# Optimization experiments

Measured on AMD Instinct MI355X. Metric: run time of the kernel, lower is better.

Reference implementation:

```python
import jax, jax.numpy as jnp
import numpy as np

N_QUBITS = 12
N_LAYERS = 6
BATCH = 256
INPUT_DIM = 256
OUT_DIM = 64
PI = float(np.pi)


def _ry_mat(a):
    # a: scalar or (B,) real angle -> (...,2,2) complex64 RY matrix
    c, s = jnp.cos(a * 0.5), jnp.sin(a * 0.5)
    return jnp.stack([jnp.stack([c, -s], -1), jnp.stack([s, c], -1)], -2).astype(jnp.complex64)


def _rz_mat(a):
    # diag(e^{-i a/2}, e^{+i a/2})
    em = jnp.exp(-0.5j * a.astype(jnp.complex64))
    ep = jnp.exp(0.5j * a.astype(jnp.complex64))
    z = jnp.zeros_like(em)
    return jnp.stack([jnp.stack([em, z], -1), jnp.stack([z, ep], -1)], -2)


def _apply_1q(state, U, w):
    # shared (2,2) gate on wire w; state: (B, 2, ..., 2)
    s = jnp.moveaxis(state, w + 1, -1)
    s = jnp.einsum('ij,b...j->b...i', U, s)
    return jnp.moveaxis(s, -1, w + 1)


def _apply_1q_batched(state, U, w):
    # per-sample (B,2,2) gate on wire w
    s = jnp.moveaxis(state, w + 1, -1)
    s = jnp.einsum('bij,b...j->b...i', U, s)
    return jnp.moveaxis(s, -1, w + 1)


def _cnot(state, c, t):
    s0 = jnp.take(state, 0, axis=c + 1)
    s1 = jnp.take(state, 1, axis=c + 1)
    t_ax = t + 1 if t < c else t  # target axis index after removing control axis
    s1 = jnp.flip(s1, axis=t_ax)
    return jnp.stack([s0, s1], axis=c + 1)


def _cz(state, c, t):
    idx = [slice(None)] * (N_QUBITS + 1)
    idx[c + 1] = 1
    idx[t + 1] = 1
    return state.at[tuple(idx)].multiply(-1.0)


def _run_circuit(xq, q_weights):
    # xq: (B, n_qubits) in [-1,1]; forward passes xq*pi, circuit multiplies by pi again
    B = xq.shape[0]
    enc = xq * (PI * PI)
    state = jnp.zeros((B, 2 ** N_QUBITS), jnp.complex64).at[:, 0].set(1.0)
    state = state.reshape((B,) + (2,) * N_QUBITS)
    for i in range(N_QUBITS):
        state = _apply_1q_batched(state, _ry_mat(enc[:, i]), i)
    w = q_weights.reshape(N_LAYERS, N_QUBITS, 3)
    for layer in range(N_LAYERS):
        for i in range(N_QUBITS):
            # PennyLane order: RZ(w0) then RY(w1) then RZ(w2) -> U = RZ2 @ RY1 @ RZ0
            U = _rz_mat(w[layer, i, 2]) @ _ry_mat(w[layer, i, 1]) @ _rz_mat(w[layer, i, 0])
            state = _apply_1q(state, U, i)
        for i in range(N_QUBITS):
            state = _cnot(state, i, (i + 1) % N_QUBITS)
        if layer % 2 == 0 and layer < N_LAYERS - 1:
            for i in range(N_QUBITS):
                state = _apply_1q_batched(state, _ry_mat(enc[:, i] * 0.5), i)
        if layer % 2 == 1:
            for i in range(0, N_QUBITS - 2, 2):
                state = _cz(state, i, i + 2)
    # PauliZ expectation on wires 0,1,2
    p = (state.real ** 2 + state.imag ** 2).reshape(B, 2, 2, 2, -1).sum(-1)  # (B,2,2,2)
    z0 = (p[:, 0] - p[:, 1]).sum((-1, -2))
    z1 = (p[:, :, 0] - p[:, :, 1]).sum((-1, -2))
    z2 = (p[:, :, :, 0] - p[:, :, :, 1]).sum((-1, -2))
    return jnp.stack([z0, z1, z2], -1)  # (B, 3) float32


def _layernorm(h, g, b, eps=1e-5):
    mu = h.mean(-1, keepdims=True)
    var = ((h - mu) ** 2).mean(-1, keepdims=True)
    return (h - mu) * jax.lax.rsqrt(var + eps) * g + b


def _forward(x, W1, b1, g_ln, b_ln, W2, b2, W3, b3, q_weights, W4, b4, W5, b5):
    gelu = lambda t: jax.nn.gelu(t, approximate=False)
    h = gelu(x @ W1.T + b1)
    h = _layernorm(h, g_ln, b_ln)
    h = gelu(h @ W2.T + b2)
    xq = jnp.tanh(h @ W3.T + b3)  # (B, n_qubits)
    q = _run_circuit(xq, q_weights)  # (B, 3)
    return gelu(q @ W4.T + b4) @ W5.T + b5  # (B, OUT_DIM)


def setup_inputs() -> dict:
    key = jax.random.key(0)
    ks = jax.random.split(key, 8)
    rn = lambda k, shape, s=0.05: (jax.random.normal(k, shape) * s).astype(jnp.float32)
    return {
        'x': jax.random.normal(ks[0], (BATCH, INPUT_DIM), jnp.float32),
        'W1': rn(ks[1], (128, INPUT_DIM)), 'b1': jnp.zeros(128, jnp.float32),
        'g_ln': jnp.ones(128, jnp.float32), 'b_ln': jnp.zeros(128, jnp.float32),
        'W2': rn(ks[2], (64, 128)), 'b2': jnp.zeros(64, jnp.float32),
        'W3': rn(ks[3], (N_QUBITS, 64)), 'b3': jnp.zeros(N_QUBITS, jnp.float32),
        'q_weights': (jax.random.normal(ks[4], (N_LAYERS * N_QUBITS * 3,)) * 0.1).astype(jnp.float32),
        'W4': rn(ks[5], (32, 3)), 'b4': jnp.zeros(32, jnp.float32),
        'W5': rn(ks[6], (OUT_DIM, 32)), 'b5': jnp.zeros(OUT_DIM, jnp.float32),
    }


def reference(x, W1, b1, g_ln, b_ln, W2, b2, W3, b3, q_weights, W4, b4, W5, b5):
    return _forward(x, W1, b1, g_ln, b_ln, W2, b2, W3, b3, q_weights, W4, b4, W5, b5)
```

## Files before the change

### kernel.cpp

```cpp
#include <hip/hip_runtime.h>
#include <math.h>

#define NQ   12
#define NL   6
#define BATCH 256
#define NT   512
#define PI2  9.869604401089358f

typedef float v2f __attribute__((ext_vector_type(2)));

__device__ __forceinline__ float geluf(float x) {
    return 0.5f * x * (1.0f + erff(x * 0.70710678118654752f));
}

__device__ __forceinline__ int Pad(int x) { return x + (x >> 4) + (x >> 8); }

__device__ __forceinline__ int gmap(int j) {
    return ((j ^ (j >> 1)) & 0x3FF)
         | ((((j >> 10) ^ (j >> 11) ^ j) & 1) << 10)
         | ((((j >> 11) ^ j) & 1) << 11);
}

__device__ __forceinline__ v2f mk2(float a, float b) { v2f r; r.x = a; r.y = b; return r; }
__device__ __forceinline__ v2f spl(float s)          { v2f r; r.x = s; r.y = s; return r; }
__device__ __forceinline__ v2f swn(v2f x)            { v2f r; r.x = -x.y; r.y = x.x; return r; }
__device__ __forceinline__ v2f cml(v2f u, v2f x)          { return spl(u.x) * x + spl(u.y) * swn(x); }
__device__ __forceinline__ v2f cma(v2f u, v2f x, v2f acc) { return acc + spl(u.x) * x + spl(u.y) * swn(x); }

__device__ __forceinline__ void bf(v2f& x0, v2f& x1, const v2f* U) {
    v2f o0 = cma(U[1], x1, cml(U[0], x0));
    v2f o1 = cma(U[3], x1, cml(U[2], x0));
    x0 = o0; x1 = o1;
}

__device__ __forceinline__ void gate_reg(v2f* a, const v2f* U, int bit) {
    #pragma unroll
    for (int m = 0; m < 8; m++) {
        if (m & bit) continue;
        bf(a[m], a[m | bit], U);
    }
}

template<int CTRL>
__device__ __forceinline__ v2f dppv(v2f v) {
    int x = __builtin_amdgcn_update_dpp(0, __float_as_int(v.x), CTRL, 0xF, 0xF, true);
    int y = __builtin_amdgcn_update_dpp(0, __float_as_int(v.y), CTRL, 0xF, 0xF, true);
    return mk2(__int_as_float(x), __int_as_float(y));
}
template<int CTRL>
__device__ __forceinline__ void gate_dpp(v2f* a, const v2f* U, bool sel) {
    const v2f cA = sel ? U[3] : U[0];
    const v2f cB = sel ? U[2] : U[1];
    #pragma unroll
    for (int m = 0; m < 8; m++) {
        v2f v = dppv<CTRL>(a[m]);
        a[m] = cma(cB, v, cml(cA, a[m]));
    }
}

__global__ __launch_bounds__(NT)
void qpu_kernel(const float* __restrict__ x,   const float* __restrict__ W1, const float* __restrict__ b1,
                const float* __restrict__ g_ln, const float* __restrict__ b_ln,
                const float* __restrict__ W2,  const float* __restrict__ b2,
                const float* __restrict__ W3,  const float* __restrict__ b3,
                const float* __restrict__ qw,  const float* __restrict__ W4, const float* __restrict__ b4,
                const float* __restrict__ W5,  const float* __restrict__ b5,
                float* __restrict__ out)
{
    __shared__ v2f   bufA[4368];
    __shared__ v2f   bufB[4368];
    __shared__ v2f   Um[NL * NQ * 4];
    __shared__ float xs[256];
    __shared__ float pr[1280];
    __shared__ float h1n[128];
    __shared__ float h2s[64];
    __shared__ float xqs[NQ];
    __shared__ float musd[2];
    __shared__ float qv[3];
    __shared__ float h4s[32];
    __shared__ float zred[8][3];

    const int t = threadIdx.x;
    const int b = blockIdx.x;

    if (t < 256) xs[t] = x[b * 256 + t];
    __syncthreads();

    {
        const int o = t >> 2, part = t & 3;
        const float4* w  = (const float4*)(W1 + o * 256) + part * 16;
        const float*  xp = xs + part * 64;
        float a0 = 0.f, a1 = 0.f, a2 = 0.f, a3 = 0.f;
        #pragma unroll
        for (int k = 0; k < 16; k++) {
            float4 wv = w[k];
            a0 = fmaf(wv.x, xp[4 * k + 0], a0);
            a1 = fmaf(wv.y, xp[4 * k + 1], a1);
            a2 = fmaf(wv.z, xp[4 * k + 2], a2);
            a3 = fmaf(wv.w, xp[4 * k + 3], a3);
        }
        pr[o * 5 + part] = (a0 + a1) + (a2 + a3);
    }
    __syncthreads();
    if (t < 128) {
        float s = pr[t * 5 + 0] + pr[t * 5 + 1] + pr[t * 5 + 2] + pr[t * 5 + 3];
        h1n[t] = geluf(s + b1[t]);
    }
    __syncthreads();

    if (t < 64) {
        float v0 = h1n[t], v1 = h1n[t + 64];
        float s1 = v0 + v1;
        float s2 = fmaf(v0, v0, v1 * v1);
        #pragma unroll
        for (int off = 32; off > 0; off >>= 1) {
            s1 += __shfl_down(s1, off);
            s2 += __shfl_down(s2, off);
        }
        if (t == 0) {
            float mu  = s1 * (1.f / 128.f);
            float var = s2 * (1.f / 128.f) - mu * mu;
            musd[0] = mu;
            musd[1] = rsqrtf(var + 1e-5f);
        }
    }
    __syncthreads();
    if (t < 128) h1n[t] = (h1n[t] - musd[0]) * musd[1] * g_ln[t] + b_ln[t];
    __syncthreads();

    {
        const int o = t >> 3, part = t & 7;
        if (o < 64) {
            const float4* w  = (const float4*)(W2 + o * 128) + part * 4;
            const float*  hp = h1n + part * 16;
            float a0 = 0.f, a1 = 0.f, a2 = 0.f, a3 = 0.f;
            #pragma unroll
            for (int k = 0; k < 4; k++) {
                float4 wv = w[k];
                a0 = fmaf(wv.x, hp[4 * k + 0], a0);
                a1 = fmaf(wv.y, hp[4 * k + 1], a1);
                a2 = fmaf(wv.z, hp[4 * k + 2], a2);
                a3 = fmaf(wv.w, hp[4 * k + 3], a3);
            }
            pr[o * 9 + part] = (a0 + a1) + (a2 + a3);
        }
    }
    __syncthreads();
    if (t < 64) {
        float s = 0.f;
        #pragma unroll
        for (int k = 0; k < 8; k++) s += pr[t * 9 + k];
        h2s[t] = geluf(s + b2[t]);
    }
    __syncthreads();

    if (t < 96) {
        const int o = t >> 3, part = t & 7;
        const float4* w  = (const float4*)(W3 + o * 64) + part * 2;
        const float*  hp = h2s + part * 8;
        float4 w0 = w[0], w1 = w[1];
        float s = 0.f;
        s = fmaf(w0.x, hp[0], s); s = fmaf(w0.y, hp[1], s);
        s = fmaf(w0.z, hp[2], s); s = fmaf(w0.w, hp[3], s);
        s = fmaf(w1.x, hp[4], s); s = fmaf(w1.y, hp[5], s);
        s = fmaf(w1.z, hp[6], s); s = fmaf(w1.w, hp[7], s);
        pr[o * 9 + part] = s;
    }
    __syncthreads();
    if (t < NQ) {
        float s = 0.f;
        #pragma unroll
        for (int k = 0; k < 8; k++) s += pr[t * 9 + k];
        xqs[t] = tanhf(s + b3[t]);
    }
    __syncthreads();

    if (t < NL * NQ) {
        const int l = t / NQ;
        const int i = t % NQ;
        float a  = qw[t * 3 + 0];
        float bb = qw[t * 3 + 1];
        float c  = qw[t * 3 + 2];
        float sb, cb;   sincosf(0.5f * bb, &sb, &cb);
        float apc = 0.5f * (a + c), amc = 0.5f * (a - c);
        float sapc, capc; sincosf(apc, &sapc, &capc);
        float samc, camc; sincosf(amc, &samc, &camc);
        float u00x =  cb * capc, u00y = -cb * sapc;
        float u01x = -sb * camc, u01y = -sb * samc;
        float u10x =  sb * camc, u10y = -sb * samc;
        float u11x =  cb * capc, u11y =  cb * sapc;

        float theta = 0.f;
        bool merge = false;
        if (l == 0)      { theta = xqs[i] * PI2;        merge = true; }
        else if (l & 1)  { theta = xqs[i] * PI2 * 0.5f; merge = true; }
        if (merge) {
            float sy, cy; sincosf(0.5f * theta, &sy, &cy);
            float m00x = u00x * cy + u01x * sy, m00y = u00y * cy + u01y * sy;
            float m01x = -u00x * sy + u01x * cy, m01y = -u00y * sy + u01y * cy;
            float m10x = u10x * cy + u11x * sy, m10y = u10y * cy + u11y * sy;
            float m11x = -u10x * sy + u11x * cy, m11y = -u10y * sy + u11y * cy;
            u00x = m00x; u00y = m00y; u01x = m01x; u01y = m01y;
            u10x = m10x; u10y = m10y; u11x = m11x; u11y = m11y;
        }
        Um[t * 4 + 0] = mk2(u00x, u00y);
        Um[t * 4 + 1] = mk2(u01x, u01y);
        Um[t * 4 + 2] = mk2(u10x, u10y);
        Um[t * 4 + 3] = mk2(u11x, u11y);
    }
    __syncthreads();

    const int PwA = 8 * t + (t >> 1) + (t >> 5);
    const int s0  = (((t     ) & 1) << 9) | (((t >> 1) & 1) << 10) | ((t >> 2) & 1)
                  | (((t >> 3) & 1) << 11) | (((t >> 4) & 1) << 1)  | (((t >> 5) & 1) << 2)
                  | (((t >> 6) & 1) << 3)  | (((t >> 7) & 1) << 4)  | (((t >> 8) & 1) << 6);
    const int Ps  = Pad(s0);
    const int g8  = gmap(8 * t);

    v2f a[8];
    {
        v2f common = Um[(11 - 3) * 4 + ((g8 >> 3) & 1) * 2];
        #pragma unroll
        for (int k = 4; k <= 9; k++) {
            common = cml(common, Um[(11 - k) * 4 + ((g8 >> k) & 1) * 2]);
        }
        #pragma unroll
        for (int m = 0; m < 8; m++) {
            const int gmc = (m ^ (m >> 1)) | ((m & 1) ? 0xC00 : 0);
            const int g = g8 ^ gmc;
            v2f v = common;
            v = cml(v, Um[11 * 4 + ((g     ) & 1) * 2]);
            v = cml(v, Um[10 * 4 + ((g >> 1) & 1) * 2]);
            v = cml(v, Um[ 9 * 4 + ((g >> 2) & 1) * 2]);
            v = cml(v, Um[ 1 * 4 + ((g >> 10) & 1) * 2]);
            v = cml(v, Um[ 0 * 4 + ((g >> 11) & 1) * 2]);
            a[m] = v;
        }
    }

    const bool d1 = t & 1, d2 = t & 2, d8 = t & 8;
    #pragma unroll 1
    for (int l = 1; l < NL; l++) {
        const v2f* UL = &Um[l * NQ * 4];

        gate_reg(a, &UL[11 * 4], 1);
        gate_reg(a, &UL[10 * 4], 2);
        gate_reg(a, &UL[ 9 * 4], 4);
        gate_dpp<0xB1> (a, &UL[8 * 4], d1);
        gate_dpp<0x4E> (a, &UL[7 * 4], d2);
        gate_dpp<0x128>(a, &UL[5 * 4], d8);

        #pragma unroll
        for (int m = 0; m < 8; m++) bufB[PwA + m] = a[m];
        __syncthreads();
        #pragma unroll
        for (int m = 0; m < 8; m++) {
            const int dm = 34 * (m & 1) + 136 * ((m >> 1) & 1) + 273 * ((m >> 2) & 1);
            a[m] = bufB[Ps + dm];
        }

        gate_reg(a, &UL[6 * 4], 1);
        gate_reg(a, &UL[4 * 4], 2);
        gate_reg(a, &UL[3 * 4], 4);
        gate_dpp<0xB1> (a, &UL[2 * 4], d1);
        gate_dpp<0x4E> (a, &UL[1 * 4], d2);
        gate_dpp<0x128>(a, &UL[0 * 4], d8);

        if (l < NL - 1) {
            #pragma unroll
            for (int m = 0; m < 8; m++) {
                const int dm = 34 * (m & 1) + 136 * ((m >> 1) & 1) + 273 * ((m >> 2) & 1);
                bufA[Ps + dm] = a[m];
            }
            __syncthreads();
            const bool czl = (l == 1) || (l == 3);
            #pragma unroll
            for (int m = 0; m < 8; m++) {
                const int gmc = (m ^ (m >> 1)) | ((m & 1) ? 0xC00 : 0);
                const int g = g8 ^ gmc;
                v2f v = bufA[Pad(g)];
                const int j = 8 * t + m;
                if (czl && (__popc(j & (j << 2) & 0xAA8) & 1)) v = -v;
                a[m] = v;
            }
        }
    }

    float alt = 0.f, tot = 0.f;
    #pragma unroll
    for (int m = 0; m < 8; m++) {
        float p = a[m].x * a[m].x + a[m].y * a[m].y;
        tot += p;
        alt += (__popc(m) & 1) ? -p : p;
    }
    float z0 = (__popc(t & 0x1F7) & 1) ? -alt : alt;
    float z1 = (__popc(t & 0x00A) & 1) ? -tot : tot;
    float z2 = (__popc(t & 0x00B) & 1) ? -tot : tot;

    #pragma unroll
    for (int off = 32; off > 0; off >>= 1) {
        z0 += __shfl_down(z0, off);
        z1 += __shfl_down(z1, off);
        z2 += __shfl_down(z2, off);
    }
    if ((t & 63) == 0) {
        zred[t >> 6][0] = z0;
        zred[t >> 6][1] = z1;
        zred[t >> 6][2] = z2;
    }
    __syncthreads();
    if (t == 0) {
        float q0 = 0.f, q1 = 0.f, q2 = 0.f;
        #pragma unroll
        for (int w = 0; w < 8; w++) {
            q0 += zred[w][0]; q1 += zred[w][1]; q2 += zred[w][2];
        }
        qv[0] = q0; qv[1] = q1; qv[2] = q2;
    }
    __syncthreads();

    if (t < 32) {
        float h = b4[t];
        h = fmaf(qv[0], W4[t * 3 + 0], h);
        h = fmaf(qv[1], W4[t * 3 + 1], h);
        h = fmaf(qv[2], W4[t * 3 + 2], h);
        h4s[t] = geluf(h);
    }
    __syncthreads();
    if (t < 64) {
        float acc = b5[t];
        #pragma unroll
        for (int h = 0; h < 32; h++) acc = fmaf(h4s[h], W5[t * 32 + h], acc);
        out[b * 64 + t] = acc;
    }
}

extern "C" void kernel_launch(void* const* d_in, const int* in_sizes, int n_in,
                              void* d_out, int out_size, void* d_ws, size_t ws_size,
                              hipStream_t stream) {
    (void)in_sizes; (void)n_in; (void)d_ws; (void)ws_size; (void)out_size;
    const float* x    = (const float*)d_in[0];
    const float* W1   = (const float*)d_in[1];
    const float* b1   = (const float*)d_in[2];
    const float* g_ln = (const float*)d_in[3];
    const float* b_ln = (const float*)d_in[4];
    const float* W2   = (const float*)d_in[5];
    const float* b2   = (const float*)d_in[6];
    const float* W3   = (const float*)d_in[7];
    const float* b3   = (const float*)d_in[8];
    const float* qw   = (const float*)d_in[9];
    const float* W4   = (const float*)d_in[10];
    const float* b4   = (const float*)d_in[11];
    const float* W5   = (const float*)d_in[12];
    const float* b5   = (const float*)d_in[13];
    float* out = (float*)d_out;

    qpu_kernel<<<BATCH, NT, 0, stream>>>(x, W1, b1, g_ln, b_ln, W2, b2,
                                         W3, b3, qw, W4, b4, W5, b5, out);
}
```

Baseline: 108.3 us.

## Double threads to 1024 with 4 amplitudes per thread in split real/imag layout

```diff
diff --git a/kernel.cpp b/kernel.cpp
--- a/kernel.cpp
+++ b/kernel.cpp
@@ -4,7 +4,7 @@
 #define NQ   12
 #define NL   6
 #define BATCH 256
-#define NT   512
+#define NT   1024
 #define PI2  9.869604401089358f
 
 typedef float v2f __attribute__((ext_vector_type(2)));
@@ -21,41 +21,16 @@
          | ((((j >> 11) ^ j) & 1) << 11);
 }
 
-__device__ __forceinline__ v2f mk2(float a, float b) { v2f r; r.x = a; r.y = b; return r; }
-__device__ __forceinline__ v2f spl(float s)          { v2f r; r.x = s; r.y = s; return r; }
-__device__ __forceinline__ v2f swn(v2f x)            { v2f r; r.x = -x.y; r.y = x.x; return r; }
-__device__ __forceinline__ v2f cml(v2f u, v2f x)          { return spl(u.x) * x + spl(u.y) * swn(x); }
-__device__ __forceinline__ v2f cma(v2f u, v2f x, v2f acc) { return acc + spl(u.x) * x + spl(u.y) * swn(x); }
-
-__device__ __forceinline__ void bf(v2f& x0, v2f& x1, const v2f* U) {
-    v2f o0 = cma(U[1], x1, cml(U[0], x0));
-    v2f o1 = cma(U[3], x1, cml(U[2], x0));
-    x0 = o0; x1 = o1;
-}
-
-__device__ __forceinline__ void gate_reg(v2f* a, const v2f* U, int bit) {
-    #pragma unroll
-    for (int m = 0; m < 8; m++) {
-        if (m & bit) continue;
-        bf(a[m], a[m | bit], U);
-    }
-}
-
 template<int CTRL>
 __device__ __forceinline__ v2f dppv(v2f v) {
     int x = __builtin_amdgcn_update_dpp(0, __float_as_int(v.x), CTRL, 0xF, 0xF, true);
     int y = __builtin_amdgcn_update_dpp(0, __float_as_int(v.y), CTRL, 0xF, 0xF, true);
-    return mk2(__int_as_float(x), __int_as_float(y));
-}
-template<int CTRL>
-__device__ __forceinline__ void gate_dpp(v2f* a, const v2f* U, bool sel) {
-    const v2f cA = sel ? U[3] : U[0];
-    const v2f cB = sel ? U[2] : U[1];
-    #pragma unroll
-    for (int m = 0; m < 8; m++) {
-        v2f v = dppv<CTRL>(a[m]);
-        a[m] = cma(cB, v, cml(cA, a[m]));
-    }
+    v2f r; r.x = __int_as_float(x); r.y = __int_as_float(y); return r;
+}
+__device__ __forceinline__ v2f swz4(v2f v) {
+    int x = __builtin_amdgcn_ds_swizzle(__float_as_int(v.x), 0x101F);
+    int y = __builtin_amdgcn_ds_swizzle(__float_as_int(v.y), 0x101F);
+    v2f r; r.x = __int_as_float(x); r.y = __int_as_float(y); return r;
 }
 
 __global__ __launch_bounds__(NT)
@@ -67,18 +42,18 @@
                 const float* __restrict__ W5,  const float* __restrict__ b5,
                 float* __restrict__ out)
 {
-    __shared__ v2f   bufA[4368];
-    __shared__ v2f   bufB[4368];
-    __shared__ v2f   Um[NL * NQ * 4];
-    __shared__ float xs[256];
-    __shared__ float pr[1280];
-    __shared__ float h1n[128];
-    __shared__ float h2s[64];
-    __shared__ float xqs[NQ];
-    __shared__ float musd[2];
-    __shared__ float qv[3];
-    __shared__ float h4s[32];
-    __shared__ float zred[8][3];
+    __shared__ float2 bufA[4368];
+    __shared__ float2 bufB[4368];
+    __shared__ float  Um8[NL * NQ * 8];
+    __shared__ float  xs[256];
+    __shared__ float  pr[1280];
+    __shared__ float  h1n[128];
+    __shared__ float  h2s[64];
+    __shared__ float  xqs[NQ];
+    __shared__ float  musd[2];
+    __shared__ float  qv[3];
+    __shared__ float  h4s[32];
+    __shared__ float  zred[16][3];
 
     const int t = threadIdx.x;
     const int b = blockIdx.x;
@@ -87,23 +62,25 @@
     __syncthreads();
 
     {
-        const int o = t >> 2, part = t & 3;
-        const float4* w  = (const float4*)(W1 + o * 256) + part * 16;
-        const float*  xp = xs + part * 64;
+        const int o = t >> 3, part = t & 7;
+        const float4* w  = (const float4*)(W1 + o * 256) + part * 8;
+        const float*  xp = xs + part * 32;
         float a0 = 0.f, a1 = 0.f, a2 = 0.f, a3 = 0.f;
         #pragma unroll
-        for (int k = 0; k < 16; k++) {
+        for (int k = 0; k < 8; k++) {
             float4 wv = w[k];
             a0 = fmaf(wv.x, xp[4 * k + 0], a0);
             a1 = fmaf(wv.y, xp[4 * k + 1], a1);
             a2 = fmaf(wv.z, xp[4 * k + 2], a2);
             a3 = fmaf(wv.w, xp[4 * k + 3], a3);
         }
-        pr[o * 5 + part] = (a0 + a1) + (a2 + a3);
+        pr[o * 9 + part] = (a0 + a1) + (a2 + a3);
     }
     __syncthreads();
     if (t < 128) {
-        float s = pr[t * 5 + 0] + pr[t * 5 + 1] + pr[t * 5 + 2] + pr[t * 5 + 3];
+        float s = 0.f;
+        #pragma unroll
+        for (int k = 0; k < 8; k++) s += pr[t * 9 + k];
         h1n[t] = geluf(s + b1[t]);
     }
     __syncthreads();
@@ -128,22 +105,20 @@
     if (t < 128) h1n[t] = (h1n[t] - musd[0]) * musd[1] * g_ln[t] + b_ln[t];
     __syncthreads();
 
-    {
+    if (t < 512) {
         const int o = t >> 3, part = t & 7;
-        if (o < 64) {
-            const float4* w  = (const float4*)(W2 + o * 128) + part * 4;
-            const float*  hp = h1n + part * 16;
-            float a0 = 0.f, a1 = 0.f, a2 = 0.f, a3 = 0.f;
-            #pragma unroll
-            for (int k = 0; k < 4; k++) {
-                float4 wv = w[k];
-                a0 = fmaf(wv.x, hp[4 * k + 0], a0);
-                a1 = fmaf(wv.y, hp[4 * k + 1], a1);
-                a2 = fmaf(wv.z, hp[4 * k + 2], a2);
-                a3 = fmaf(wv.w, hp[4 * k + 3], a3);
-            }
-            pr[o * 9 + part] = (a0 + a1) + (a2 + a3);
-        }
+        const float4* w  = (const float4*)(W2 + o * 128) + part * 4;
+        const float*  hp = h1n + part * 16;
+        float a0 = 0.f, a1 = 0.f, a2 = 0.f, a3 = 0.f;
+        #pragma unroll
+        for (int k = 0; k < 4; k++) {
+            float4 wv = w[k];
+            a0 = fmaf(wv.x, hp[4 * k + 0], a0);
+            a1 = fmaf(wv.y, hp[4 * k + 1], a1);
+            a2 = fmaf(wv.z, hp[4 * k + 2], a2);
+            a3 = fmaf(wv.w, hp[4 * k + 3], a3);
+        }
+        pr[o * 9 + part] = (a0 + a1) + (a2 + a3);
     }
     __syncthreads();
     if (t < 64) {
@@ -196,106 +171,172 @@
         else if (l & 1)  { theta = xqs[i] * PI2 * 0.5f; merge = true; }
         if (merge) {
             float sy, cy; sincosf(0.5f * theta, &sy, &cy);
-            float m00x = u00x * cy + u01x * sy, m00y = u00y * cy + u01y * sy;
+            float m00x = u00x * cy + u01x * sy,  m00y = u00y * cy + u01y * sy;
             float m01x = -u00x * sy + u01x * cy, m01y = -u00y * sy + u01y * cy;
-            float m10x = u10x * cy + u11x * sy, m10y = u10y * cy + u11y * sy;
+            float m10x = u10x * cy + u11x * sy,  m10y = u10y * cy + u11y * sy;
             float m11x = -u10x * sy + u11x * cy, m11y = -u10y * sy + u11y * cy;
             u00x = m00x; u00y = m00y; u01x = m01x; u01y = m01y;
             u10x = m10x; u10y = m10y; u11x = m11x; u11y = m11y;
         }
-        Um[t * 4 + 0] = mk2(u00x, u00y);
-        Um[t * 4 + 1] = mk2(u01x, u01y);
-        Um[t * 4 + 2] = mk2(u10x, u10y);
-        Um[t * 4 + 3] = mk2(u11x, u11y);
-    }
-    __syncthreads();
-
-    const int PwA = 8 * t + (t >> 1) + (t >> 5);
-    const int s0  = (((t     ) & 1) << 9) | (((t >> 1) & 1) << 10) | ((t >> 2) & 1)
-                  | (((t >> 3) & 1) << 11) | (((t >> 4) & 1) << 1)  | (((t >> 5) & 1) << 2)
-                  | (((t >> 6) & 1) << 3)  | (((t >> 7) & 1) << 4)  | (((t >> 8) & 1) << 6);
+        float* d = &Um8[t * 8];
+        d[0] = u00x; d[1] = u00y; d[2] = u01x; d[3] = u01y;
+        d[4] = u10x; d[5] = u10y; d[6] = u11x; d[7] = u11y;
+    }
+    __syncthreads();
+
+    const int PwA = 4 * t + (t >> 2) + (t >> 6);
+    const int s0  = ((t >> 4) & 3) | (((t >> 6) & 15) << 2) | ((t & 15) << 8);
     const int Ps  = Pad(s0);
-    const int g8  = gmap(8 * t);
-
-    v2f a[8];
+    const int g4t = gmap(4 * t);
+    const int pg0 = Pad(g4t);
+    const int pg1 = Pad(g4t ^ 0xC01);
+    const int pg2 = Pad(g4t ^ 0x003);
+    const int pg3 = Pad(g4t ^ 0xC02);
+    const int  czb = __popc(t & (t >> 2) & 0xAA) & 1;
+    const float sA = czb ? -1.f : 1.f;
+    const float sB = (czb ^ ((t >> 1) & 1)) ? -1.f : 1.f;
+    const bool d1 = t & 1, d2 = t & 2, d4 = t & 4, d8 = t & 8;
+
+    v2f R01, R23, I01, I23;
     {
-        v2f common = Um[(11 - 3) * 4 + ((g8 >> 3) & 1) * 2];
-        #pragma unroll
-        for (int k = 4; k <= 9; k++) {
-            common = cml(common, Um[(11 - k) * 4 + ((g8 >> k) & 1) * 2]);
-        }
-        #pragma unroll
-        for (int m = 0; m < 8; m++) {
-            const int gmc = (m ^ (m >> 1)) | ((m & 1) ? 0xC00 : 0);
-            const int g = g8 ^ gmc;
-            v2f v = common;
-            v = cml(v, Um[11 * 4 + ((g     ) & 1) * 2]);
-            v = cml(v, Um[10 * 4 + ((g >> 1) & 1) * 2]);
-            v = cml(v, Um[ 9 * 4 + ((g >> 2) & 1) * 2]);
-            v = cml(v, Um[ 1 * 4 + ((g >> 10) & 1) * 2]);
-            v = cml(v, Um[ 0 * 4 + ((g >> 11) & 1) * 2]);
-            a[m] = v;
-        }
-    }
-
-    const bool d1 = t & 1, d2 = t & 2, d8 = t & 8;
+        float cr, ci;
+        {
+            const float* u = &Um8[9 * 8 + (((g4t >> 2) & 1) << 2)];
+            cr = u[0]; ci = u[1];
+        }
+        #pragma unroll
+        for (int k = 3; k <= 9; k++) {
+            const float* u = &Um8[(11 - k) * 8 + (((g4t >> k) & 1) << 2)];
+            float nr = cr * u[0] - ci * u[1];
+            float ni = cr * u[1] + ci * u[0];
+            cr = nr; ci = ni;
+        }
+        const int GM[4] = {0, 0xC01, 0x003, 0xC02};
+        float vr[4], vi[4];
+        #pragma unroll
+        for (int m = 0; m < 4; m++) {
+            const int g = g4t ^ GM[m];
+            float rr = cr, ii = ci;
+            const float* u0 = &Um8[11 * 8 + ((g & 1) << 2)];
+            const float* u1 = &Um8[10 * 8 + (((g >> 1) & 1) << 2)];
+            const float* ua = &Um8[ 1 * 8 + (((g >> 10) & 1) << 2)];
+            const float* ub = &Um8[ 0 * 8 + (((g >> 11) & 1) << 2)];
+            float nr, ni;
+            nr = rr * u0[0] - ii * u0[1]; ni = rr * u0[1] + ii * u0[0]; rr = nr; ii = ni;
+            nr = rr * u1[0] - ii * u1[1]; ni = rr * u1[1] + ii * u1[0]; rr = nr; ii = ni;
+            nr = rr * ua[0] - ii * ua[1]; ni = rr * ua[1] + ii * ua[0]; rr = nr; ii = ni;
+            nr = rr * ub[0] - ii * ub[1]; ni = rr * ub[1] + ii * ub[0]; rr = nr; ii = ni;
+            vr[m] = rr; vi[m] = ii;
+        }
+        R01.x = vr[0]; R01.y = vr[1]; R23.x = vr[2]; R23.y = vr[3];
+        I01.x = vi[0]; I01.y = vi[1]; I23.x = vi[2]; I23.y = vi[3];
+    }
+
     #pragma unroll 1
     for (int l = 1; l < NL; l++) {
-        const v2f* UL = &Um[l * NQ * 4];
-
-        gate_reg(a, &UL[11 * 4], 1);
-        gate_reg(a, &UL[10 * 4], 2);
-        gate_reg(a, &UL[ 9 * 4], 4);
-        gate_dpp<0xB1> (a, &UL[8 * 4], d1);
-        gate_dpp<0x4E> (a, &UL[7 * 4], d2);
-        gate_dpp<0x128>(a, &UL[5 * 4], d8);
-
-        #pragma unroll
-        for (int m = 0; m < 8; m++) bufB[PwA + m] = a[m];
+        const float* UL = &Um8[l * NQ * 8];
+
+        {
+            const float* u = &UL[11 * 8];
+            float r0 = R01.x, i0 = I01.x, r1 = R01.y, i1 = I01.y;
+            R01.x = u[0]*r0 - u[1]*i0 + u[2]*r1 - u[3]*i1;
+            I01.x = u[0]*i0 + u[1]*r0 + u[2]*i1 + u[3]*r1;
+            R01.y = u[4]*r0 - u[5]*i0 + u[6]*r1 - u[7]*i1;
+            I01.y = u[4]*i0 + u[5]*r0 + u[6]*i1 + u[7]*r1;
+            r0 = R23.x; i0 = I23.x; r1 = R23.y; i1 = I23.y;
+            R23.x = u[0]*r0 - u[1]*i0 + u[2]*r1 - u[3]*i1;
+            I23.x = u[0]*i0 + u[1]*r0 + u[2]*i1 + u[3]*r1;
+            R23.y = u[4]*r0 - u[5]*i0 + u[6]*r1 - u[7]*i1;
+            I23.y = u[4]*i0 + u[5]*r0 + u[6]*i1 + u[7]*r1;
+        }
+        {
+            const float* u = &UL[10 * 8];
+            v2f r0 = u[0]*R01 - u[1]*I01 + u[2]*R23 - u[3]*I23;
+            v2f i0 = u[0]*I01 + u[1]*R01 + u[2]*I23 + u[3]*R23;
+            v2f r1 = u[4]*R01 - u[5]*I01 + u[6]*R23 - u[7]*I23;
+            v2f i1 = u[4]*I01 + u[5]*R01 + u[6]*I23 + u[7]*R23;
+            R01 = r0; I01 = i0; R23 = r1; I23 = i1;
+        }
+        #define LANE_GATE(PERM, Q, SEL) do {                                  \
+            const float* u = &UL[(Q) * 8];                                    \
+            float cAx = (SEL) ? u[6] : u[0], cAy = (SEL) ? u[7] : u[1];       \
+            float cBx = (SEL) ? u[4] : u[2], cBy = (SEL) ? u[5] : u[3];       \
+            v2f vR0 = PERM(R01), vI0 = PERM(I01);                             \
+            v2f vR1 = PERM(R23), vI1 = PERM(I23);                             \
+            v2f nR0 = cAx*R01 - cAy*I01 + cBx*vR0 - cBy*vI0;                  \
+            v2f nI0 = cAx*I01 + cAy*R01 + cBx*vI0 + cBy*vR0;                  \
+            v2f nR1 = cAx*R23 - cAy*I23 + cBx*vR1 - cBy*vI1;                  \
+            v2f nI1 = cAx*I23 + cAy*R23 + cBx*vI1 + cBy*vR1;                  \
+            R01 = nR0; I01 = nI0; R23 = nR1; I23 = nI1; } while (0)
+
+        LANE_GATE(dppv<0xB1>,  9, d1);
+        LANE_GATE(dppv<0x4E>,  8, d2);
+        LANE_GATE(swz4,        7, d4);
+        LANE_GATE(dppv<0x128>, 6, d8);
+
+        bufB[PwA + 0] = make_float2(R01.x, I01.x);
+        bufB[PwA + 1] = make_float2(R01.y, I01.y);
+        bufB[PwA + 2] = make_float2(R23.x, I23.x);
+        bufB[PwA + 3] = make_float2(R23.y, I23.y);
         __syncthreads();
-        #pragma unroll
-        for (int m = 0; m < 8; m++) {
-            const int dm = 34 * (m & 1) + 136 * ((m >> 1) & 1) + 273 * ((m >> 2) & 1);
-            a[m] = bufB[Ps + dm];
-        }
-
-        gate_reg(a, &UL[6 * 4], 1);
-        gate_reg(a, &UL[4 * 4], 2);
-        gate_reg(a, &UL[3 * 4], 4);
-        gate_dpp<0xB1> (a, &UL[2 * 4], d1);
-        gate_dpp<0x4E> (a, &UL[1 * 4], d2);
-        gate_dpp<0x128>(a, &UL[0 * 4], d8);
+        {
+            float2 v0 = bufB[Ps], v1 = bufB[Ps + 68], v2 = bufB[Ps + 136], v3 = bufB[Ps + 204];
+            R01.x = v0.x; I01.x = v0.y; R01.y = v1.x; I01.y = v1.y;
+            R23.x = v2.x; I23.x = v2.y; R23.y = v3.x; I23.y = v3.y;
+        }
+
+        {
+            const float* u = &UL[5 * 8];
+            float r0 = R01.x, i0 = I01.x, r1 = R01.y, i1 = I01.y;
+            R01.x = u[0]*r0 - u[1]*i0 + u[2]*r1 - u[3]*i1;
+            I01.x = u[0]*i0 + u[1]*r0 + u[2]*i1 + u[3]*r1;
+            R01.y = u[4]*r0 - u[5]*i0 + u[6]*r1 - u[7]*i1;
+            I01.y = u[4]*i0 + u[5]*r0 + u[6]*i1 + u[7]*r1;
+            r0 = R23.x; i0 = I23.x; r1 = R23.y; i1 = I23.y;
+            R23.x = u[0]*r0 - u[1]*i0 + u[2]*r1 - u[3]*i1;
+            I23.x = u[0]*i0 + u[1]*r0 + u[2]*i1 + u[3]*r1;
+            R23.y = u[4]*r0 - u[5]*i0 + u[6]*r1 - u[7]*i1;
+            I23.y = u[4]*i0 + u[5]*r0 + u[6]*i1 + u[7]*r1;
+        }
+        {
+            const float* u = &UL[4 * 8];
+            v2f r0 = u[0]*R01 - u[1]*I01 + u[2]*R23 - u[3]*I23;
+            v2f i0 = u[0]*I01 + u[1]*R01 + u[2]*I23 + u[3]*R23;
+            v2f r1 = u[4]*R01 - u[5]*I01 + u[6]*R23 - u[7]*I23;
+            v2f i1 = u[4]*I01 + u[5]*R01 + u[6]*I23 + u[7]*R23;
+            R01 = r0; I01 = i0; R23 = r1; I23 = i1;
+        }
+        LANE_GATE(dppv<0xB1>,  3, d1);
+        LANE_GATE(dppv<0x4E>,  2, d2);
+        LANE_GATE(swz4,        1, d4);
+        LANE_GATE(dppv<0x128>, 0, d8);
+        #undef LANE_GATE
 
         if (l < NL - 1) {
-            #pragma unroll
-            for (int m = 0; m < 8; m++) {
-                const int dm = 34 * (m & 1) + 136 * ((m >> 1) & 1) + 273 * ((m >> 2) & 1);
-                bufA[Ps + dm] = a[m];
+            bufA[Ps +   0] = make_float2(R01.x, I01.x);
+            bufA[Ps +  68] = make_float2(R01.y, I01.y);
+            bufA[Ps + 136] = make_float2(R23.x, I23.x);
+            bufA[Ps + 204] = make_float2(R23.y, I23.y);
+            __syncthreads();
+            float2 w0 = bufA[pg0], w1 = bufA[pg1], w2 = bufA[pg2], w3 = bufA[pg3];
+            if ((l == 1) || (l == 3)) {
+                w0.x *= sA; w0.y *= sA; w1.x *= sA; w1.y *= sA;
+                w2.x *= sB; w2.y *= sB; w3.x *= sB; w3.y *= sB;
             }
-            __syncthreads();
-            const bool czl = (l == 1) || (l == 3);
-            #pragma unroll
-            for (int m = 0; m < 8; m++) {
-                const int gmc = (m ^ (m >> 1)) | ((m & 1) ? 0xC00 : 0);
-                const int g = g8 ^ gmc;
-                v2f v = bufA[Pad(g)];
-                const int j = 8 * t + m;
-                if (czl && (__popc(j & (j << 2) & 0xAA8) & 1)) v = -v;
-                a[m] = v;
-            }
-        }
-    }
-
-    float alt = 0.f, tot = 0.f;
-    #pragma unroll
-    for (int m = 0; m < 8; m++) {
-        float p = a[m].x * a[m].x + a[m].y * a[m].y;
-        tot += p;
-        alt += (__popc(m) & 1) ? -p : p;
-    }
-    float z0 = (__popc(t & 0x1F7) & 1) ? -alt : alt;
-    float z1 = (__popc(t & 0x00A) & 1) ? -tot : tot;
-    float z2 = (__popc(t & 0x00B) & 1) ? -tot : tot;
+            R01.x = w0.x; I01.x = w0.y; R01.y = w1.x; I01.y = w1.y;
+            R23.x = w2.x; I23.x = w2.y; R23.y = w3.x; I23.y = w3.y;
+        }
+    }
+
+    float p0 = R01.x * R01.x + I01.x * I01.x;
+    float p1 = R01.y * R01.y + I01.y * I01.y;
+    float p2 = R23.x * R23.x + I23.x * I23.x;
+    float p3 = R23.y * R23.y + I23.y * I23.y;
+    float alt = (p0 - p1) - (p2 - p3);
+    float tot = (p0 + p1) + (p2 + p3);
+    float z0 = (__popc(t & 0x3F7) & 1) ? -alt : alt;
+    float z1 = (__popc(t & 0x00C) & 1) ? -tot : tot;
+    float z2 = (__popc(t & 0x00E) & 1) ? -tot : tot;
 
     #pragma unroll
     for (int off = 32; off > 0; off >>= 1) {
@@ -312,7 +353,7 @@
     if (t == 0) {
         float q0 = 0.f, q1 = 0.f, q2 = 0.f;
         #pragma unroll
-        for (int w = 0; w < 8; w++) {
+        for (int w = 0; w < 16; w++) {
             q0 += zred[w][0]; q1 += zred[w][1]; q2 += zred[w][2];
         }
         qv[0] = q0; qv[1] = q1; qv[2] = q2;
```

New measurement: 103.1 us. 4.8% less time.

## Store state as split real/imag packed vectors and prelayout gate matrices

Applied to the files above, without the earlier changes.

```diff
diff --git a/kernel.cpp b/kernel.cpp
--- a/kernel.cpp
+++ b/kernel.cpp
@@ -21,41 +21,16 @@
          | ((((j >> 11) ^ j) & 1) << 11);
 }
 
-__device__ __forceinline__ v2f mk2(float a, float b) { v2f r; r.x = a; r.y = b; return r; }
-__device__ __forceinline__ v2f spl(float s)          { v2f r; r.x = s; r.y = s; return r; }
-__device__ __forceinline__ v2f swn(v2f x)            { v2f r; r.x = -x.y; r.y = x.x; return r; }
-__device__ __forceinline__ v2f cml(v2f u, v2f x)          { return spl(u.x) * x + spl(u.y) * swn(x); }
-__device__ __forceinline__ v2f cma(v2f u, v2f x, v2f acc) { return acc + spl(u.x) * x + spl(u.y) * swn(x); }
-
-__device__ __forceinline__ void bf(v2f& x0, v2f& x1, const v2f* U) {
-    v2f o0 = cma(U[1], x1, cml(U[0], x0));
-    v2f o1 = cma(U[3], x1, cml(U[2], x0));
-    x0 = o0; x1 = o1;
-}
-
-__device__ __forceinline__ void gate_reg(v2f* a, const v2f* U, int bit) {
-    #pragma unroll
-    for (int m = 0; m < 8; m++) {
-        if (m & bit) continue;
-        bf(a[m], a[m | bit], U);
-    }
+__device__ __forceinline__ int sigma(int x) {
+    return ((x & 0x1E) << 6) | ((x & 0x780) >> 6)
+         | ((x & 0x41) << 5) | ((x & 0x820) >> 5);
 }
 
 template<int CTRL>
 __device__ __forceinline__ v2f dppv(v2f v) {
     int x = __builtin_amdgcn_update_dpp(0, __float_as_int(v.x), CTRL, 0xF, 0xF, true);
     int y = __builtin_amdgcn_update_dpp(0, __float_as_int(v.y), CTRL, 0xF, 0xF, true);
-    return mk2(__int_as_float(x), __int_as_float(y));
-}
-template<int CTRL>
-__device__ __forceinline__ void gate_dpp(v2f* a, const v2f* U, bool sel) {
-    const v2f cA = sel ? U[3] : U[0];
-    const v2f cB = sel ? U[2] : U[1];
-    #pragma unroll
-    for (int m = 0; m < 8; m++) {
-        v2f v = dppv<CTRL>(a[m]);
-        a[m] = cma(cB, v, cml(cA, a[m]));
-    }
+    v2f r; r.x = __int_as_float(x); r.y = __int_as_float(y); return r;
 }
 
 __global__ __launch_bounds__(NT)
@@ -67,18 +42,19 @@
                 const float* __restrict__ W5,  const float* __restrict__ b5,
                 float* __restrict__ out)
 {
-    __shared__ v2f   bufA[4368];
-    __shared__ v2f   bufB[4368];
-    __shared__ v2f   Um[NL * NQ * 4];
-    __shared__ float xs[256];
-    __shared__ float pr[1280];
-    __shared__ float h1n[128];
-    __shared__ float h2s[64];
-    __shared__ float xqs[NQ];
-    __shared__ float musd[2];
-    __shared__ float qv[3];
-    __shared__ float h4s[32];
-    __shared__ float zred[8][3];
+    __shared__ float2 bufA[4368];
+    __shared__ float2 bufB[4368];
+    __shared__ float  Umr[5 * 12 * 8];
+    __shared__ float4 L0c[12];
+    __shared__ float  xs[256];
+    __shared__ float  pr[1280];
+    __shared__ float  h1n[128];
+    __shared__ float  h2s[64];
+    __shared__ float  xqs[NQ];
+    __shared__ float  musd[2];
+    __shared__ float  qv[3];
+    __shared__ float  h4s[32];
+    __shared__ float  zred[8][3];
 
     const int t = threadIdx.x;
     const int b = blockIdx.x;
@@ -130,20 +106,18 @@
 
     {
         const int o = t >> 3, part = t & 7;
-        if (o < 64) {
-            const float4* w  = (const float4*)(W2 + o * 128) + part * 4;
-            const float*  hp = h1n + part * 16;
-            float a0 = 0.f, a1 = 0.f, a2 = 0.f, a3 = 0.f;
-            #pragma unroll
-            for (int k = 0; k < 4; k++) {
-                float4 wv = w[k];
-                a0 = fmaf(wv.x, hp[4 * k + 0], a0);
-                a1 = fmaf(wv.y, hp[4 * k + 1], a1);
-                a2 = fmaf(wv.z, hp[4 * k + 2], a2);
-                a3 = fmaf(wv.w, hp[4 * k + 3], a3);
-            }
-            pr[o * 9 + part] = (a0 + a1) + (a2 + a3);
-        }
+        const float4* w  = (const float4*)(W2 + o * 128) + part * 4;
+        const float*  hp = h1n + part * 16;
+        float a0 = 0.f, a1 = 0.f, a2 = 0.f, a3 = 0.f;
+        #pragma unroll
+        for (int k = 0; k < 4; k++) {
+            float4 wv = w[k];
+            a0 = fmaf(wv.x, hp[4 * k + 0], a0);
+            a1 = fmaf(wv.y, hp[4 * k + 1], a1);
+            a2 = fmaf(wv.z, hp[4 * k + 2], a2);
+            a3 = fmaf(wv.w, hp[4 * k + 3], a3);
+        }
+        pr[o * 9 + part] = (a0 + a1) + (a2 + a3);
     }
     __syncthreads();
     if (t < 64) {
@@ -196,103 +170,198 @@
         else if (l & 1)  { theta = xqs[i] * PI2 * 0.5f; merge = true; }
         if (merge) {
             float sy, cy; sincosf(0.5f * theta, &sy, &cy);
-            float m00x = u00x * cy + u01x * sy, m00y = u00y * cy + u01y * sy;
+            float m00x = u00x * cy + u01x * sy,  m00y = u00y * cy + u01y * sy;
             float m01x = -u00x * sy + u01x * cy, m01y = -u00y * sy + u01y * cy;
-            float m10x = u10x * cy + u11x * sy, m10y = u10y * cy + u11y * sy;
+            float m10x = u10x * cy + u11x * sy,  m10y = u10y * cy + u11y * sy;
             float m11x = -u10x * sy + u11x * cy, m11y = -u10y * sy + u11y * cy;
             u00x = m00x; u00y = m00y; u01x = m01x; u01y = m01y;
             u10x = m10x; u10y = m10y; u11x = m11x; u11y = m11y;
         }
-        Um[t * 4 + 0] = mk2(u00x, u00y);
-        Um[t * 4 + 1] = mk2(u01x, u01y);
-        Um[t * 4 + 2] = mk2(u10x, u10y);
-        Um[t * 4 + 3] = mk2(u11x, u11y);
+        if (l == 0) {
+            L0c[i] = make_float4(u00x, u00y, u10x, u10y);
+        } else {
+            float* d = &Umr[((l - 1) * 12 + i) * 8];
+            if (i == 11 || i == 6) {
+                d[0] = u00x; d[1] = u10x; d[2] = u00y; d[3] = u10y;
+                d[4] = u01x; d[5] = u11x; d[6] = u01y; d[7] = u11y;
+            } else if (i == 10 || i == 9 || i == 4 || i == 3) {
+                d[0] = u00x; d[1] = u00y; d[2] = u01x; d[3] = u01y;
+                d[4] = u10x; d[5] = u10y; d[6] = u11x; d[7] = u11y;
+            } else {
+                d[0] = u00x; d[1] = u00y; d[2] = u01x; d[3] = u01y;
+                d[4] = u11x; d[5] = u11y; d[6] = u10x; d[7] = u10y;
+            }
+        }
     }
     __syncthreads();
 
     const int PwA = 8 * t + (t >> 1) + (t >> 5);
-    const int s0  = (((t     ) & 1) << 9) | (((t >> 1) & 1) << 10) | ((t >> 2) & 1)
-                  | (((t >> 3) & 1) << 11) | (((t >> 4) & 1) << 1)  | (((t >> 5) & 1) << 2)
-                  | (((t >> 6) & 1) << 3)  | (((t >> 7) & 1) << 4)  | (((t >> 8) & 1) << 6);
-    const int Ps  = Pad(s0);
-    const int g8  = gmap(8 * t);
-
-    v2f a[8];
+    const int s8t = sigma(8 * t);
+    const int Ps  = Pad(s8t);
+    const int SD[8] = {0, 34, 136, 170, 273, 307, 409, 443};
+    const int g8t = gmap(8 * t);
+    const int GMm[8] = {0, 0xC01, 3, 0xC02, 6, 0xC07, 5, 0xC04};
+    int   qm[8];
+    float czm[8];
+    #pragma unroll
+    for (int m = 0; m < 8; m++) {
+        qm[m] = Pad(g8t ^ GMm[m]);
+        const int j = 8 * t + m;
+        czm[m] = (__popc(j & (j << 2) & 0xAA8) & 1) ? -1.f : 1.f;
+    }
+    const bool t0 = t & 1, t1 = t & 2, t3 = t & 8;
+
+    v2f R[4], I[4];
     {
-        v2f common = Um[(11 - 3) * 4 + ((g8 >> 3) & 1) * 2];
+        float cr, ci;
+        {
+            const float4 f = L0c[8];
+            const bool bit = (g8t >> 3) & 1;
+            cr = bit ? f.z : f.x; ci = bit ? f.w : f.y;
+        }
         #pragma unroll
         for (int k = 4; k <= 9; k++) {
-            common = cml(common, Um[(11 - k) * 4 + ((g8 >> k) & 1) * 2]);
+            const float4 f = L0c[11 - k];
+            const bool bit = (g8t >> k) & 1;
+            const float fr = bit ? f.z : f.x, fi = bit ? f.w : f.y;
+            const float nr = cr * fr - ci * fi;
+            const float ni = cr * fi + ci * fr;
+            cr = nr; ci = ni;
         }
         #pragma unroll
         for (int m = 0; m < 8; m++) {
-            const int gmc = (m ^ (m >> 1)) | ((m & 1) ? 0xC00 : 0);
-            const int g = g8 ^ gmc;
-            v2f v = common;
-            v = cml(v, Um[11 * 4 + ((g     ) & 1) * 2]);
-            v = cml(v, Um[10 * 4 + ((g >> 1) & 1) * 2]);
-            v = cml(v, Um[ 9 * 4 + ((g >> 2) & 1) * 2]);
-            v = cml(v, Um[ 1 * 4 + ((g >> 10) & 1) * 2]);
-            v = cml(v, Um[ 0 * 4 + ((g >> 11) & 1) * 2]);
-            a[m] = v;
-        }
-    }
-
-    const bool d1 = t & 1, d2 = t & 2, d8 = t & 8;
+            const int g = g8t ^ GMm[m];
+            float rr = cr, ii = ci;
+            const int KB[5] = {0, 1, 2, 10, 11};
+            #pragma unroll
+            for (int q = 0; q < 5; q++) {
+                const int k = KB[q];
+                const float4 f = L0c[11 - k];
+                const bool bit = (g >> k) & 1;
+                const float fr = bit ? f.z : f.x, fi = bit ? f.w : f.y;
+                const float nr = rr * fr - ii * fi;
+                const float ni = rr * fi + ii * fr;
+                rr = nr; ii = ni;
+            }
+            if (m & 1) { R[m >> 1].y = rr; I[m >> 1].y = ii; }
+            else       { R[m >> 1].x = rr; I[m >> 1].x = ii; }
+        }
+    }
+
+    #define GATE_IP(BASE) do {                                                \
+        const float4 A  = *(const float4*)(BASE);                             \
+        const float4 Bq = *(const float4*)((BASE) + 4);                       \
+        v2f CAr, CAi, CBr, CBi;                                               \
+        CAr.x = A.x;  CAr.y = A.y;  CAi.x = A.z;  CAi.y = A.w;                \
+        CBr.x = Bq.x; CBr.y = Bq.y; CBi.x = Bq.z; CBi.y = Bq.w;               \
+        _Pragma("unroll")                                                     \
+        for (int k = 0; k < 4; k++) {                                         \
+            v2f rxx, ryy, ixx, iyy;                                           \
+            rxx.x = R[k].x; rxx.y = R[k].x; ryy.x = R[k].y; ryy.y = R[k].y;   \
+            ixx.x = I[k].x; ixx.y = I[k].x; iyy.x = I[k].y; iyy.y = I[k].y;   \
+            v2f nR = CAr * rxx - CAi * ixx + CBr * ryy - CBi * iyy;           \
+            v2f nI = CAi * rxx + CAr * ixx + CBi * ryy + CBr * iyy;           \
+            R[k] = nR; I[k] = nI;                                             \
+        } } while (0)
+
+    #define GATE_CP_PAIR(c0, c1, A0, B0) do {                                 \
+        v2f Ra = R[A0], Ia = I[A0], Rb = R[B0], Ib = I[B0];                   \
+        R[A0] = c0.x * Ra - c0.y * Ia + c0.z * Rb - c0.w * Ib;                \
+        I[A0] = c0.y * Ra + c0.x * Ia + c0.w * Rb + c0.z * Ib;                \
+        R[B0] = c1.x * Ra - c1.y * Ia + c1.z * Rb - c1.w * Ib;                \
+        I[B0] = c1.y * Ra + c1.x * Ia + c1.w * Rb + c1.z * Ib;                \
+        } while (0)
+
+    #define GATE_CP(BASE, A0, B0, A1, B1) do {                                \
+        const float4 c0 = *(const float4*)(BASE);                             \
+        const float4 c1 = *(const float4*)((BASE) + 4);                       \
+        GATE_CP_PAIR(c0, c1, A0, B0);                                         \
+        GATE_CP_PAIR(c0, c1, A1, B1);                                         \
+        } while (0)
+
+    #define GATE_DPP(BASE, SEL, CTRL) do {                                    \
+        const float4 c = *(const float4*)((BASE) + ((SEL) ? 4 : 0));          \
+        _Pragma("unroll")                                                     \
+        for (int k = 0; k < 4; k++) {                                         \
+            v2f vR = dppv<CTRL>(R[k]);                                        \
+            v2f vI = dppv<CTRL>(I[k]);                                        \
+            v2f nR = c.x * R[k] - c.y * I[k] + c.z * vR - c.w * vI;           \
+            v2f nI = c.y * R[k] + c.x * I[k] + c.w * vR + c.z * vI;           \
+            R[k] = nR; I[k] = nI;                                             \
+        } } while (0)
+
     #pragma unroll 1
     for (int l = 1; l < NL; l++) {
-        const v2f* UL = &Um[l * NQ * 4];
-
-        gate_reg(a, &UL[11 * 4], 1);
-        gate_reg(a, &UL[10 * 4], 2);
-        gate_reg(a, &UL[ 9 * 4], 4);
-        gate_dpp<0xB1> (a, &UL[8 * 4], d1);
-        gate_dpp<0x4E> (a, &UL[7 * 4], d2);
-        gate_dpp<0x128>(a, &UL[5 * 4], d8);
-
-        #pragma unroll
-        for (int m = 0; m < 8; m++) bufB[PwA + m] = a[m];
-        __syncthreads();
-        #pragma unroll
-        for (int m = 0; m < 8; m++) {
-            const int dm = 34 * (m & 1) + 136 * ((m >> 1) & 1) + 273 * ((m >> 2) & 1);
-            a[m] = bufB[Ps + dm];
-        }
-
-        gate_reg(a, &UL[6 * 4], 1);
-        gate_reg(a, &UL[4 * 4], 2);
-        gate_reg(a, &UL[3 * 4], 4);
-        gate_dpp<0xB1> (a, &UL[2 * 4], d1);
-        gate_dpp<0x4E> (a, &UL[1 * 4], d2);
-        gate_dpp<0x128>(a, &UL[0 * 4], d8);
+        const float* UL = &Umr[(l - 1) * 96];
+
+        GATE_IP(UL + 11 * 8);
+        GATE_CP(UL + 10 * 8, 0, 1, 2, 3);
+        GATE_CP(UL +  9 * 8, 0, 2, 1, 3);
+        GATE_DPP(UL + 8 * 8, t0, 0xB1);
+        GATE_DPP(UL + 7 * 8, t1, 0x4E);
+        GATE_DPP(UL + 5 * 8, t3, 0x128);
+
+        {
+            float2* w = &bufA[PwA];
+            w[0] = make_float2(R[0].x, I[0].x);
+            w[1] = make_float2(R[0].y, I[0].y);
+            w[2] = make_float2(R[1].x, I[1].x);
+            w[3] = make_float2(R[1].y, I[1].y);
+            w[4] = make_float2(R[2].x, I[2].x);
+            w[5] = make_float2(R[2].y, I[2].y);
+            w[6] = make_float2(R[3].x, I[3].x);
+            w[7] = make_float2(R[3].y, I[3].y);
+            __syncthreads();
+            #pragma unroll
+            for (int m = 0; m < 8; m++) {
+                const float2 v = bufA[Ps + SD[m]];
+                if (m & 1) { R[m >> 1].y = v.x; I[m >> 1].y = v.y; }
+                else       { R[m >> 1].x = v.x; I[m >> 1].x = v.y; }
+            }
+        }
+
+        GATE_IP(UL + 6 * 8);
+        GATE_CP(UL + 4 * 8, 0, 1, 2, 3);
+        GATE_CP(UL + 3 * 8, 0, 2, 1, 3);
+        GATE_DPP(UL + 2 * 8, t0, 0xB1);
+        GATE_DPP(UL + 1 * 8, t1, 0x4E);
+        GATE_DPP(UL + 0 * 8, t3, 0x128);
 
         if (l < NL - 1) {
             #pragma unroll
             for (int m = 0; m < 8; m++) {
-                const int dm = 34 * (m & 1) + 136 * ((m >> 1) & 1) + 273 * ((m >> 2) & 1);
-                bufA[Ps + dm] = a[m];
+                float2 v;
+                if (m & 1) { v.x = R[m >> 1].y; v.y = I[m >> 1].y; }
+                else       { v.x = R[m >> 1].x; v.y = I[m >> 1].x; }
+                bufB[Ps + SD[m]] = v;
             }
             __syncthreads();
             const bool czl = (l == 1) || (l == 3);
             #pragma unroll
             for (int m = 0; m < 8; m++) {
-                const int gmc = (m ^ (m >> 1)) | ((m & 1) ? 0xC00 : 0);
-                const int g = g8 ^ gmc;
-                v2f v = bufA[Pad(g)];
-                const int j = 8 * t + m;
-                if (czl && (__popc(j & (j << 2) & 0xAA8) & 1)) v = -v;
-                a[m] = v;
+                float2 v = bufB[qm[m]];
+                if (czl) { v.x *= czm[m]; v.y *= czm[m]; }
+                if (m & 1) { R[m >> 1].y = v.x; I[m >> 1].y = v.y; }
+                else       { R[m >> 1].x = v.x; I[m >> 1].x = v.y; }
             }
         }
     }
-
-    float alt = 0.f, tot = 0.f;
-    #pragma unroll
-    for (int m = 0; m < 8; m++) {
-        float p = a[m].x * a[m].x + a[m].y * a[m].y;
-        tot += p;
-        alt += (__popc(m) & 1) ? -p : p;
-    }
+    #undef GATE_IP
+    #undef GATE_CP
+    #undef GATE_CP_PAIR
+    #undef GATE_DPP
+
+    float p[8];
+    p[0] = R[0].x * R[0].x + I[0].x * I[0].x;
+    p[1] = R[0].y * R[0].y + I[0].y * I[0].y;
+    p[2] = R[1].x * R[1].x + I[1].x * I[1].x;
+    p[3] = R[1].y * R[1].y + I[1].y * I[1].y;
+    p[4] = R[2].x * R[2].x + I[2].x * I[2].x;
+    p[5] = R[2].y * R[2].y + I[2].y * I[2].y;
+    p[6] = R[3].x * R[3].x + I[3].x * I[3].x;
+    p[7] = R[3].y * R[3].y + I[3].y * I[3].y;
+    float alt = (p[0] - p[1] - p[2] + p[3]) - (p[4] - p[5] - p[6] + p[7]);
+    float tot = (p[0] + p[1] + p[2] + p[3]) + (p[4] + p[5] + p[6] + p[7]);
     float z0 = (__popc(t & 0x1F7) & 1) ? -alt : alt;
     float z1 = (__popc(t & 0x00A) & 1) ? -tot : tot;
     float z2 = (__popc(t & 0x00B) & 1) ? -tot : tot;
```

Result: faster. 103.0 us (-4.9%).
